# Performance work log

Measured on AMD Instinct MI355X. Metric: run time of the kernel, lower is better.

Reference implementation:

```python
import jax, jax.numpy as jnp
import numpy as np

B, L, ENC_DIM, DEC_DIM, ATTN_DIM = 64, 2048, 1024, 1024, 512


def setup_inputs() -> dict:
    key = jax.random.key(0)
    ks = jax.random.split(key, 8)
    s_enc = 1.0 / np.sqrt(ENC_DIM)
    s_dec = 1.0 / np.sqrt(DEC_DIM)
    s_full = 1.0 / np.sqrt(ATTN_DIM)
    return {
        "encoder_out": jax.random.normal(ks[0], (B, L, ENC_DIM), jnp.float32),
        "decoder_hidden": jax.random.normal(ks[1], (B, DEC_DIM), jnp.float32),
        "We_w": jax.random.uniform(ks[2], (ENC_DIM, ATTN_DIM), jnp.float32, -s_enc, s_enc),
        "We_b": jax.random.uniform(ks[3], (ATTN_DIM,), jnp.float32, -s_enc, s_enc),
        "Wd_w": jax.random.uniform(ks[4], (DEC_DIM, ATTN_DIM), jnp.float32, -s_dec, s_dec),
        "Wd_b": jax.random.uniform(ks[5], (ATTN_DIM,), jnp.float32, -s_dec, s_dec),
        "Wf_w": jax.random.uniform(ks[6], (ATTN_DIM,), jnp.float32, -s_full, s_full),
        "Wf_b": jax.random.uniform(ks[7], (), jnp.float32, -s_full, s_full),
    }


def reference(encoder_out, decoder_hidden, We_w, We_b, Wd_w, Wd_b, Wf_w, Wf_b):
    # enc_attn: [B, L, A]; dec_attn: [B, A]
    enc_attn = jnp.einsum("ble,ea->bla", encoder_out, We_w) + We_b
    dec_attn = decoder_hidden @ Wd_w + Wd_b
    # additive score -> scalar per (B, L)
    hidden = jax.nn.relu(enc_attn + dec_attn[:, None, :])
    attn = jnp.einsum("bla,a->bl", hidden, Wf_w) + Wf_b
    alpha = jax.nn.softmax(attn, axis=1)  # over sequence dim
    weighted = jnp.einsum("ble,bl->be", encoder_out, alpha)
    return (weighted, alpha)
```

## Files before the change

### kernel.cpp

```cpp
#include <hip/hip_runtime.h>
#include <stdint.h>

#define B_BATCH 64
#define L_SEQ 2048
#define E_DIM 1024
#define A_DIM 512

typedef __attribute__((ext_vector_type(4))) float f32x4;
typedef __attribute__((ext_vector_type(8))) short bf16x8;
typedef __attribute__((ext_vector_type(2))) unsigned int u32x2;
typedef __attribute__((ext_vector_type(4))) unsigned int u32x4;

__device__ __forceinline__ unsigned short f2bf(float f) {
  unsigned u = __float_as_uint(f);
  u = (u + 0x7fffu + ((u >> 16) & 1u)) >> 16;
  return (unsigned short)u;
}

__device__ __forceinline__ u32x2 packbf(f32x4 v) {
  u32x2 r;
  r.x = (unsigned)f2bf(v.x) | ((unsigned)f2bf(v.y) << 16);
  r.y = (unsigned)f2bf(v.z) | ((unsigned)f2bf(v.w) << 16);
  return r;
}

__device__ __forceinline__ void gload_lds16(const void* g, void* l) {
  __builtin_amdgcn_global_load_lds(
      (const __attribute__((address_space(1))) unsigned int*)(uintptr_t)g,
      (__attribute__((address_space(3))) unsigned int*)(unsigned)(uintptr_t)l,
      16, 0, 0);
}

#define BCHUNK 32768
#define BUFB 24576
#define ABASE 16384

__global__ void prep_we_kernel(const float* __restrict__ We, char* __restrict__ wsB) {
  int t = blockIdx.x * 256 + threadIdx.x;
  int n = t & 511;
  int kgl = t >> 9;
  int e0 = kgl * 4;
  int kb = e0 >> 5;
  int kg = (e0 >> 2) & 7;
  unsigned lo = (unsigned)f2bf(We[(size_t)(e0 + 0) * A_DIM + n]) |
                ((unsigned)f2bf(We[(size_t)(e0 + 1) * A_DIM + n]) << 16);
  unsigned hi = (unsigned)f2bf(We[(size_t)(e0 + 2) * A_DIM + n]) |
                ((unsigned)f2bf(We[(size_t)(e0 + 3) * A_DIM + n]) << 16);
  u32x2 val; val.x = lo; val.y = hi;
  int slot = (kg & 3) ^ ((n >> 1) & 3);
  *(u32x2*)(wsB + (size_t)kb * BCHUNK + n * 64 + slot * 16 + (kg >> 2) * 8) = val;
}

__global__ void dec_comb_kernel(const float* __restrict__ dh, const float* __restrict__ Wd,
                                const float* __restrict__ Wdb, const float* __restrict__ Web,
                                float* __restrict__ dcomb) {
  __shared__ float sh[1024];
  const int b = blockIdx.x, tid = threadIdx.x;
  for (int i = tid; i < 1024; i += 256) sh[i] = dh[b * 1024 + i];
  __syncthreads();
  const int a = blockIdx.y * 256 + tid;
  float acc = Wdb[a] + Web[a];
#pragma unroll 4
  for (int e = 0; e < 1024; ++e) acc += sh[e] * Wd[(size_t)e * A_DIM + a];
  dcomb[b * A_DIM + a] = acc;
}

__global__ __launch_bounds__(256, 2) void score_gemm_kernel(
    const float* __restrict__ enc, const char* __restrict__ wsB,
    const float* __restrict__ dcomb, const float* __restrict__ wf,
    float* __restrict__ scoreOut) {
  __shared__ __align__(16) char smem[3 * BUFB];
  __shared__ float s_score[128];

  const int tid = threadIdx.x;
  const int lane = tid & 63;
  const int w = tid >> 6;
  const int g = lane >> 4;
  const int nl = lane & 15;
  const int gs = g ^ ((nl >> 1) & 3);

  const int bid = (int)blockIdx.x;
  const int lbid = (bid & 7) * 256 + (bid >> 3);
  const int split = lbid & 1;
  const int row0 = (lbid >> 1) * 128;
  const int bb = row0 >> 11;

  if (tid < 128) s_score[tid] = 0.0f;

  const float* encA = enc + (size_t)row0 * E_DIM;
  const char* bsrc = wsB + split * 16384;

  int aoff[8], boff[4];
#pragma unroll
  for (int rt = 0; rt < 8; ++rt) aoff[rt] = ABASE + (rt * 16 + nl) * 64 + gs * 16;
#pragma unroll
  for (int ct = 0; ct < 4; ++ct) boff[ct] = (w * 64 + ct * 16 + nl) * 64 + gs * 16;

  const int ar0 = tid >> 2, ac = tid & 3;
  const int aw0 = ABASE + ar0 * 64 + ((ac ^ ((ar0 >> 1) & 3)) * 16);
  const int aw1 = aw0 + 4096;
  const float* as0 = encA + (size_t)ar0 * E_DIM + ac * 4;
  const float* as1 = as0 + 64 * E_DIM;

  f32x4 acc[8][4];
#pragma unroll
  for (int rt = 0; rt < 8; ++rt)
#pragma unroll
    for (int ct = 0; ct < 4; ++ct) {
      f32x4 z = {0.f, 0.f, 0.f, 0.f};
      acc[rt][ct] = z;
    }
  f32x4 ra[2][4];

#define STAGE_B(kb_, dst_)                                                  \
  do {                                                                      \
    _Pragma("unroll") for (int c = 0; c < 4; ++c)                           \
        gload_lds16(bsrc + (size_t)(kb_)*BCHUNK + w * 4096 + c * 1024 +     \
                        lane * 16,                                          \
                    smem + (dst_) + w * 4096 + c * 1024);                   \
  } while (0)

#define LOAD_A(kb_, s_)                                 \
  do {                                                  \
    ra[s_][0] = *(const f32x4*)(as0 + (kb_)*32);        \
    ra[s_][1] = *(const f32x4*)(as0 + (kb_)*32 + 16);   \
    ra[s_][2] = *(const f32x4*)(as1 + (kb_)*32);        \
    ra[s_][3] = *(const f32x4*)(as1 + (kb_)*32 + 16);   \
  } while (0)

#define WRITE_A(s_, dst_)                                          \
  do {                                                             \
    u32x2 l0 = packbf(ra[s_][0]), h0 = packbf(ra[s_][1]);          \
    u32x2 l1 = packbf(ra[s_][2]), h1 = packbf(ra[s_][3]);          \
    u32x4 w0; w0.x = l0.x; w0.y = l0.y; w0.z = h0.x; w0.w = h0.y;  \
    u32x4 w1; w1.x = l1.x; w1.y = l1.y; w1.z = h1.x; w1.w = h1.y;  \
    *(u32x4*)(smem + (dst_) + aw0) = w0;                           \
    *(u32x4*)(smem + (dst_) + aw1) = w1;                           \
  } while (0)

#define COMPUTE(cur_)                                                        \
  do {                                                                       \
    bf16x8 bfr[4], afr[8];                                                   \
    _Pragma("unroll") for (int ct = 0; ct < 4; ++ct) bfr[ct] =               \
        *(const bf16x8*)(smem + (cur_) + boff[ct]);                          \
    _Pragma("unroll") for (int rt = 0; rt < 8; ++rt) afr[rt] =               \
        *(const bf16x8*)(smem + (cur_) + aoff[rt]);                          \
    __builtin_amdgcn_s_setprio(1);                                           \
    _Pragma("unroll") for (int rt = 0; rt < 8; ++rt)                         \
        _Pragma("unroll") for (int ct = 0; ct < 4; ++ct) acc[rt][ct] =       \
            __builtin_amdgcn_mfma_f32_16x16x32_bf16(afr[rt], bfr[ct],        \
                                                    acc[rt][ct], 0, 0, 0);   \
    __builtin_amdgcn_s_setprio(0);                                           \
  } while (0)

  LOAD_A(0, 0);
  STAGE_B(0, 0);
  LOAD_A(1, 1);
  asm volatile("s_waitcnt vmcnt(8)" ::: "memory");
  WRITE_A(0, 0);

  int b0 = 0, b1 = BUFB, b2 = 2 * BUFB;
#pragma unroll 6
  for (int t = 0; t < 30; ++t) {
    STAGE_B(t + 1, b1);
    LOAD_A(t + 2, t & 1);
    asm volatile("s_waitcnt vmcnt(8)" ::: "memory");
    WRITE_A((t + 1) & 1, b1);
    asm volatile("s_waitcnt lgkmcnt(0)" ::: "memory");
    asm volatile("s_barrier" ::: "memory");
    COMPUTE(b0);
    int tmp = b0; b0 = b1; b1 = b2; b2 = tmp;
  }
  STAGE_B(31, b1);
  asm volatile("s_waitcnt vmcnt(4)" ::: "memory");
  WRITE_A(1, b1);
  asm volatile("s_waitcnt lgkmcnt(0)" ::: "memory");
  asm volatile("s_barrier" ::: "memory");
  COMPUTE(b0);
  { int tmp = b0; b0 = b1; b1 = b2; b2 = tmp; }
  asm volatile("s_waitcnt vmcnt(0) lgkmcnt(0)" ::: "memory");
  asm volatile("s_barrier" ::: "memory");
  COMPUTE(b0);

#undef STAGE_B
#undef LOAD_A
#undef WRITE_A
#undef COMPUTE

  float db[4], wv[4];
#pragma unroll
  for (int ct = 0; ct < 4; ++ct) {
    int a = split * 256 + w * 64 + ct * 16 + nl;
    db[ct] = dcomb[bb * A_DIM + a];
    wv[ct] = wf[a];
  }
#pragma unroll
  for (int rt = 0; rt < 8; ++rt) {
#pragma unroll
    for (int r = 0; r < 4; ++r) {
      float p = 0.f;
#pragma unroll
      for (int ct = 0; ct < 4; ++ct) {
        float h = acc[rt][ct][r] + db[ct];
        h = h > 0.f ? h : 0.f;
        p += h * wv[ct];
      }
      p += __shfl_xor(p, 1);
      p += __shfl_xor(p, 2);
      p += __shfl_xor(p, 4);
      p += __shfl_xor(p, 8);
      if (nl == 0) atomicAdd(&s_score[rt * 16 + g * 4 + r], p);
    }
  }
  __syncthreads();
  if (tid < 128) atomicAdd(&scoreOut[row0 + tid], s_score[tid]);
}

__global__ void softmax_kernel(float* __restrict__ attn) {
  __shared__ float red[8];
  const int b = blockIdx.x, tid = threadIdx.x;
  float* p = attn + b * L_SEQ;
  float v[8];
  float m = -1e30f;
#pragma unroll
  for (int i = 0; i < 8; ++i) {
    v[i] = p[tid + i * 256];
    m = fmaxf(m, v[i]);
  }
#pragma unroll
  for (int off = 1; off < 64; off <<= 1) m = fmaxf(m, __shfl_xor(m, off));
  const int wid = tid >> 6;
  if ((tid & 63) == 0) red[wid] = m;
  __syncthreads();
  m = fmaxf(fmaxf(red[0], red[1]), fmaxf(red[2], red[3]));
  float s = 0.f;
#pragma unroll
  for (int i = 0; i < 8; ++i) {
    v[i] = __expf(v[i] - m);
    s += v[i];
  }
#pragma unroll
  for (int off = 1; off < 64; off <<= 1) s += __shfl_xor(s, off);
  __syncthreads();
  if ((tid & 63) == 0) red[4 + wid] = s;
  __syncthreads();
  const float inv = 1.0f / (red[4] + red[5] + red[6] + red[7]);
#pragma unroll
  for (int i = 0; i < 8; ++i) p[tid + i * 256] = v[i] * inv;
}

__global__ void weighted_kernel(const float* __restrict__ enc, const float* __restrict__ alpha,
                                float* __restrict__ outW) {
  __shared__ float sa[64];
  const int bid = blockIdx.x;
  const int b = bid >> 5, ls = bid & 31;
  const int tid = threadIdx.x;
  if (tid < 64) sa[tid] = alpha[b * L_SEQ + ls * 64 + tid];
  __syncthreads();
  const f32x4* ep = (const f32x4*)(enc + ((size_t)(b * L_SEQ + ls * 64)) * E_DIM) + tid;
  f32x4 acc = {0.f, 0.f, 0.f, 0.f};
#pragma unroll 8
  for (int il = 0; il < 64; ++il) {
    f32x4 v = ep[(size_t)il * 256];
    float al = sa[il];
    acc.x += al * v.x;
    acc.y += al * v.y;
    acc.z += al * v.z;
    acc.w += al * v.w;
  }
  float* o = outW + b * E_DIM + tid * 4;
  atomicAdd(o + 0, acc.x);
  atomicAdd(o + 1, acc.y);
  atomicAdd(o + 2, acc.z);
  atomicAdd(o + 3, acc.w);
}

extern "C" void kernel_launch(void* const* d_in, const int* in_sizes, int n_in,
                              void* d_out, int out_size, void* d_ws, size_t ws_size,
                              hipStream_t stream) {
  const float* enc = (const float*)d_in[0];
  const float* dh = (const float*)d_in[1];
  const float* WeW = (const float*)d_in[2];
  const float* WeB = (const float*)d_in[3];
  const float* WdW = (const float*)d_in[4];
  const float* WdB = (const float*)d_in[5];
  const float* WfW = (const float*)d_in[6];

  float* out = (float*)d_out;
  float* outW = out;
  float* attn = out + B_BATCH * E_DIM;

  char* wsB = (char*)d_ws;
  float* dcomb = (float*)((char*)d_ws + 32 * (size_t)BCHUNK);

  if (ws_size < 32 * (size_t)BCHUNK + (size_t)B_BATCH * A_DIM * sizeof(float)) return;

  hipMemsetAsync(out, 0, (size_t)(B_BATCH * E_DIM + B_BATCH * L_SEQ) * sizeof(float), stream);
  prep_we_kernel<<<512, 256, 0, stream>>>(WeW, wsB);
  dec_comb_kernel<<<dim3(B_BATCH, 2), 256, 0, stream>>>(dh, WdW, WdB, WeB, dcomb);
  score_gemm_kernel<<<(B_BATCH * L_SEQ) / 128 * 2, 256, 0, stream>>>(enc, wsB, dcomb, WfW, attn);
  softmax_kernel<<<B_BATCH, 256, 0, stream>>>(attn);
  weighted_kernel<<<B_BATCH * 32, 256, 0, stream>>>(enc, attn, outW);
}
```

Measured before the change: 408.5 us.

## Load B fragments directly to registers and cover full N per 512-thread block

```diff
diff --git a/kernel.cpp b/kernel.cpp
--- a/kernel.cpp
+++ b/kernel.cpp
@@ -24,31 +24,27 @@
   return r;
 }
 
-__device__ __forceinline__ void gload_lds16(const void* g, void* l) {
-  __builtin_amdgcn_global_load_lds(
-      (const __attribute__((address_space(1))) unsigned int*)(uintptr_t)g,
-      (__attribute__((address_space(3))) unsigned int*)(unsigned)(uintptr_t)l,
-      16, 0, 0);
-}
-
+#define BUFB 8192
 #define BCHUNK 32768
-#define BUFB 24576
-#define ABASE 16384
 
 __global__ void prep_we_kernel(const float* __restrict__ We, char* __restrict__ wsB) {
   int t = blockIdx.x * 256 + threadIdx.x;
-  int n = t & 511;
-  int kgl = t >> 9;
-  int e0 = kgl * 4;
-  int kb = e0 >> 5;
-  int kg = (e0 >> 2) & 7;
-  unsigned lo = (unsigned)f2bf(We[(size_t)(e0 + 0) * A_DIM + n]) |
-                ((unsigned)f2bf(We[(size_t)(e0 + 1) * A_DIM + n]) << 16);
-  unsigned hi = (unsigned)f2bf(We[(size_t)(e0 + 2) * A_DIM + n]) |
-                ((unsigned)f2bf(We[(size_t)(e0 + 3) * A_DIM + n]) << 16);
-  u32x2 val; val.x = lo; val.y = hi;
-  int slot = (kg & 3) ^ ((n >> 1) & 3);
-  *(u32x2*)(wsB + (size_t)kb * BCHUNK + n * 64 + slot * 16 + (kg >> 2) * 8) = val;
+  int lane = t & 63;
+  int colblk = (t >> 6) & 31;
+  int step = t >> 11;
+  int nl = lane & 15, g = lane >> 4;
+  int col = colblk * 16 + nl;
+  int k0 = step * 32 + 4 * g;
+  unsigned q0 = (unsigned)f2bf(We[(size_t)(k0 + 0) * A_DIM + col]) |
+                ((unsigned)f2bf(We[(size_t)(k0 + 1) * A_DIM + col]) << 16);
+  unsigned q1 = (unsigned)f2bf(We[(size_t)(k0 + 2) * A_DIM + col]) |
+                ((unsigned)f2bf(We[(size_t)(k0 + 3) * A_DIM + col]) << 16);
+  unsigned q2 = (unsigned)f2bf(We[(size_t)(k0 + 16) * A_DIM + col]) |
+                ((unsigned)f2bf(We[(size_t)(k0 + 17) * A_DIM + col]) << 16);
+  unsigned q3 = (unsigned)f2bf(We[(size_t)(k0 + 18) * A_DIM + col]) |
+                ((unsigned)f2bf(We[(size_t)(k0 + 19) * A_DIM + col]) << 16);
+  u32x4 v; v.x = q0; v.y = q1; v.z = q2; v.w = q3;
+  *(u32x4*)(wsB + (size_t)t * 16) = v;
 }
 
 __global__ void dec_comb_kernel(const float* __restrict__ dh, const float* __restrict__ Wd,
@@ -65,7 +61,7 @@
   dcomb[b * A_DIM + a] = acc;
 }
 
-__global__ __launch_bounds__(256, 2) void score_gemm_kernel(
+__global__ __launch_bounds__(512, 2) void score_gemm_kernel(
     const float* __restrict__ enc, const char* __restrict__ wsB,
     const float* __restrict__ dcomb, const float* __restrict__ wf,
     float* __restrict__ scoreOut) {
@@ -79,28 +75,22 @@
   const int nl = lane & 15;
   const int gs = g ^ ((nl >> 1) & 3);
 
-  const int bid = (int)blockIdx.x;
-  const int lbid = (bid & 7) * 256 + (bid >> 3);
-  const int split = lbid & 1;
-  const int row0 = (lbid >> 1) * 128;
+  const int row0 = (int)blockIdx.x * 128;
   const int bb = row0 >> 11;
 
   if (tid < 128) s_score[tid] = 0.0f;
 
   const float* encA = enc + (size_t)row0 * E_DIM;
-  const char* bsrc = wsB + split * 16384;
-
-  int aoff[8], boff[4];
-#pragma unroll
-  for (int rt = 0; rt < 8; ++rt) aoff[rt] = ABASE + (rt * 16 + nl) * 64 + gs * 16;
-#pragma unroll
-  for (int ct = 0; ct < 4; ++ct) boff[ct] = (w * 64 + ct * 16 + nl) * 64 + gs * 16;
-
-  const int ar0 = tid >> 2, ac = tid & 3;
-  const int aw0 = ABASE + ar0 * 64 + ((ac ^ ((ar0 >> 1) & 3)) * 16);
-  const int aw1 = aw0 + 4096;
-  const float* as0 = encA + (size_t)ar0 * E_DIM + ac * 4;
-  const float* as1 = as0 + 64 * E_DIM;
+
+  int aoff[8];
+#pragma unroll
+  for (int rt = 0; rt < 8; ++rt) aoff[rt] = (rt * 16 + nl) * 64 + gs * 16;
+
+  const int ar = tid >> 2, ag = tid & 3;
+  const int aw = ar * 64 + ((ag ^ ((ar >> 1) & 3)) * 16);
+  const float* asrc = encA + (size_t)ar * E_DIM + ag * 4;
+
+  const char* bsrc = wsB + (w * 4) * 1024 + lane * 16;
 
   f32x4 acc[8][4];
 #pragma unroll
@@ -110,87 +100,80 @@
       f32x4 z = {0.f, 0.f, 0.f, 0.f};
       acc[rt][ct] = z;
     }
-  f32x4 ra[2][4];
-
-#define STAGE_B(kb_, dst_)                                                  \
+  f32x4 ra[2][2];
+  bf16x8 bfr[2][4];
+
+#define LOAD_A(kb_, s_)                                  \
+  do {                                                   \
+    ra[s_][0] = *(const f32x4*)(asrc + (kb_) * 32);      \
+    ra[s_][1] = *(const f32x4*)(asrc + (kb_) * 32 + 16); \
+  } while (0)
+
+#define LOAD_B(kb_, s_)                                                     \
   do {                                                                      \
-    _Pragma("unroll") for (int c = 0; c < 4; ++c)                           \
-        gload_lds16(bsrc + (size_t)(kb_)*BCHUNK + w * 4096 + c * 1024 +     \
-                        lane * 16,                                          \
-                    smem + (dst_) + w * 4096 + c * 1024);                   \
-  } while (0)
-
-#define LOAD_A(kb_, s_)                                 \
-  do {                                                  \
-    ra[s_][0] = *(const f32x4*)(as0 + (kb_)*32);        \
-    ra[s_][1] = *(const f32x4*)(as0 + (kb_)*32 + 16);   \
-    ra[s_][2] = *(const f32x4*)(as1 + (kb_)*32);        \
-    ra[s_][3] = *(const f32x4*)(as1 + (kb_)*32 + 16);   \
+    _Pragma("unroll") for (int ct = 0; ct < 4; ++ct) bfr[s_][ct] =          \
+        *(const bf16x8*)(bsrc + (size_t)(kb_)*BCHUNK + ct * 1024);          \
   } while (0)
 
 #define WRITE_A(s_, dst_)                                          \
   do {                                                             \
-    u32x2 l0 = packbf(ra[s_][0]), h0 = packbf(ra[s_][1]);          \
-    u32x2 l1 = packbf(ra[s_][2]), h1 = packbf(ra[s_][3]);          \
+    u32x2 l0 = packbf(ra[s_][0]);                                  \
+    u32x2 h0 = packbf(ra[s_][1]);                                  \
     u32x4 w0; w0.x = l0.x; w0.y = l0.y; w0.z = h0.x; w0.w = h0.y;  \
-    u32x4 w1; w1.x = l1.x; w1.y = l1.y; w1.z = h1.x; w1.w = h1.y;  \
-    *(u32x4*)(smem + (dst_) + aw0) = w0;                           \
-    *(u32x4*)(smem + (dst_) + aw1) = w1;                           \
-  } while (0)
-
-#define COMPUTE(cur_)                                                        \
+    *(u32x4*)(smem + (dst_) + aw) = w0;                            \
+  } while (0)
+
+#define COMPUTE(cur_, s_)                                                    \
   do {                                                                       \
-    bf16x8 bfr[4], afr[8];                                                   \
-    _Pragma("unroll") for (int ct = 0; ct < 4; ++ct) bfr[ct] =               \
-        *(const bf16x8*)(smem + (cur_) + boff[ct]);                          \
+    bf16x8 afr[8];                                                           \
     _Pragma("unroll") for (int rt = 0; rt < 8; ++rt) afr[rt] =               \
         *(const bf16x8*)(smem + (cur_) + aoff[rt]);                          \
     __builtin_amdgcn_s_setprio(1);                                           \
     _Pragma("unroll") for (int rt = 0; rt < 8; ++rt)                         \
         _Pragma("unroll") for (int ct = 0; ct < 4; ++ct) acc[rt][ct] =       \
-            __builtin_amdgcn_mfma_f32_16x16x32_bf16(afr[rt], bfr[ct],        \
+            __builtin_amdgcn_mfma_f32_16x16x32_bf16(afr[rt], bfr[s_][ct],    \
                                                     acc[rt][ct], 0, 0, 0);   \
     __builtin_amdgcn_s_setprio(0);                                           \
   } while (0)
 
   LOAD_A(0, 0);
-  STAGE_B(0, 0);
   LOAD_A(1, 1);
-  asm volatile("s_waitcnt vmcnt(8)" ::: "memory");
+  LOAD_B(0, 0);
+  asm volatile("s_waitcnt vmcnt(6)" ::: "memory");
   WRITE_A(0, 0);
 
   int b0 = 0, b1 = BUFB, b2 = 2 * BUFB;
 #pragma unroll 6
   for (int t = 0; t < 30; ++t) {
-    STAGE_B(t + 1, b1);
     LOAD_A(t + 2, t & 1);
-    asm volatile("s_waitcnt vmcnt(8)" ::: "memory");
+    LOAD_B(t + 1, (t + 1) & 1);
+    asm volatile("s_waitcnt vmcnt(6)" ::: "memory");
     WRITE_A((t + 1) & 1, b1);
     asm volatile("s_waitcnt lgkmcnt(0)" ::: "memory");
     asm volatile("s_barrier" ::: "memory");
-    COMPUTE(b0);
+    COMPUTE(b0, t & 1);
     int tmp = b0; b0 = b1; b1 = b2; b2 = tmp;
   }
-  STAGE_B(31, b1);
+  LOAD_B(31, 1);
   asm volatile("s_waitcnt vmcnt(4)" ::: "memory");
   WRITE_A(1, b1);
   asm volatile("s_waitcnt lgkmcnt(0)" ::: "memory");
   asm volatile("s_barrier" ::: "memory");
-  COMPUTE(b0);
+  COMPUTE(b0, 0);
   { int tmp = b0; b0 = b1; b1 = b2; b2 = tmp; }
   asm volatile("s_waitcnt vmcnt(0) lgkmcnt(0)" ::: "memory");
   asm volatile("s_barrier" ::: "memory");
-  COMPUTE(b0);
-
-#undef STAGE_B
+  COMPUTE(b0, 1);
+
 #undef LOAD_A
+#undef LOAD_B
 #undef WRITE_A
 #undef COMPUTE
 
   float db[4], wv[4];
 #pragma unroll
   for (int ct = 0; ct < 4; ++ct) {
-    int a = split * 256 + w * 64 + ct * 16 + nl;
+    int a = w * 64 + ct * 16 + nl;
     db[ct] = dcomb[bb * A_DIM + a];
     wv[ct] = wf[a];
   }
@@ -213,7 +196,7 @@
     }
   }
   __syncthreads();
-  if (tid < 128) atomicAdd(&scoreOut[row0 + tid], s_score[tid]);
+  if (tid < 128) scoreOut[row0 + tid] = s_score[tid];
 }
 
 __global__ void softmax_kernel(float* __restrict__ attn) {
@@ -295,10 +278,10 @@
 
   if (ws_size < 32 * (size_t)BCHUNK + (size_t)B_BATCH * A_DIM * sizeof(float)) return;
 
-  hipMemsetAsync(out, 0, (size_t)(B_BATCH * E_DIM + B_BATCH * L_SEQ) * sizeof(float), stream);
-  prep_we_kernel<<<512, 256, 0, stream>>>(WeW, wsB);
+  hipMemsetAsync(outW, 0, (size_t)(B_BATCH * E_DIM) * sizeof(float), stream);
+  prep_we_kernel<<<256, 256, 0, stream>>>(WeW, wsB);
   dec_comb_kernel<<<dim3(B_BATCH, 2), 256, 0, stream>>>(dh, WdW, WdB, WeB, dcomb);
-  score_gemm_kernel<<<(B_BATCH * L_SEQ) / 128 * 2, 256, 0, stream>>>(enc, wsB, dcomb, WfW, attn);
+  score_gemm_kernel<<<(B_BATCH * L_SEQ) / 128, 512, 0, stream>>>(enc, wsB, dcomb, WfW, attn);
   softmax_kernel<<<B_BATCH, 256, 0, stream>>>(attn);
   weighted_kernel<<<B_BATCH * 32, 256, 0, stream>>>(enc, attn, outW);
 }
```

Result: faster. 384.5 us (-5.9%).
